# Performance work log

Measured on AMD Instinct MI355X. Metric: run time of the kernel, lower is better.

Reference implementation:

```python
import jax, jax.numpy as jnp
import numpy as np

N, E, F_IN, H, NSE, L, C, G = 50000, 800000, 128, 128, 16, 3, 10, 256


def setup_inputs() -> dict:
    key = jax.random.key(0)
    ks = jax.random.split(key, 32)
    sc = 0.05
    inp = {
        "x": jax.random.normal(ks[0], (N, F_IN), jnp.float32),
        "s": jax.random.normal(ks[1], (N, NSE), jnp.float32),
        "edge_index": jax.random.randint(ks[2], (2, E), 0, N, jnp.int64),
        "batch": jnp.sort(jax.random.randint(ks[3], (N,), 0, G, jnp.int64)),
        # pre: Linear(F_IN, H); embedding_s: Linear(NSE, H)
        "pre_w": jax.random.normal(ks[4], (F_IN, H), jnp.float32) * sc,
        "pre_b": jnp.zeros((H,), jnp.float32),
        "emb_w": jax.random.normal(ks[5], (NSE, H), jnp.float32) * sc,
        "emb_b": jnp.zeros((H,), jnp.float32),
        # per-layer GIN MLP: Linear(2H,H) -> ReLU -> Linear(H,H)
        "gin_w1": jax.random.normal(ks[6], (L, 2 * H, H), jnp.float32) * sc,
        "gin_b1": jnp.zeros((L, H), jnp.float32),
        "gin_w2": jax.random.normal(ks[7], (L, H, H), jnp.float32) * sc,
        "gin_b2": jnp.zeros((L, H), jnp.float32),
        # per-layer GCNConv(H, H)
        "gcn_w": jax.random.normal(ks[8], (L, H, H), jnp.float32) * sc,
        "gcn_b": jnp.zeros((L, H), jnp.float32),
        "whp_w": jax.random.normal(ks[9], (2 * H, H), jnp.float32) * sc,
        "whp_b": jnp.zeros((H,), jnp.float32),
        "post_w": jax.random.normal(ks[10], (H, H), jnp.float32) * sc,
        "post_b": jnp.zeros((H,), jnp.float32),
        "ro_w": jax.random.normal(ks[11], (H, C), jnp.float32) * sc,
        "ro_b": jnp.zeros((C,), jnp.float32),
    }
    return inp


def reference(x, s, edge_index, batch, pre_w, pre_b, emb_w, emb_b,
              gin_w1, gin_b1, gin_w2, gin_b2, gcn_w, gcn_b,
              whp_w, whp_b, post_w, post_b, ro_w, ro_b):
    src, dst = edge_index[0], edge_index[1]
    x = x @ pre_w + pre_b                      # [N, H]
    s = s @ emb_w + emb_b                      # [N, H]
    # GCN symmetric norm with self-loops (deg includes the +1 self loop)
    deg = jax.ops.segment_sum(jnp.ones((E,), x.dtype), dst, num_segments=N) + 1.0
    dinv = jax.lax.rsqrt(deg)                  # [N]
    enorm = (dinv[src] * dinv[dst])[:, None]   # [E, 1]
    self_norm = (dinv * dinv)[:, None]         # [N, 1]
    for i in range(L):
        xc = jnp.concatenate([x, s], axis=-1)  # [N, 2H]
        # GINConv (eps=0): nn(x_i + sum_j x_j)
        agg = jax.ops.segment_sum(xc[src], dst, num_segments=N)
        h = xc + agg
        h = jax.nn.relu(h @ gin_w1[i] + gin_b1[i]) @ gin_w2[i] + gin_b2[i]
        x = jax.nn.relu(h)                     # dropout is identity in eval mode
        # GCNConv on s stream
        hs = s @ gcn_w[i]
        sagg = jax.ops.segment_sum(hs[src] * enorm, dst, num_segments=N)
        s = jnp.tanh(sagg + hs * self_norm + gcn_b[i])
    x = jnp.concatenate([x, s], axis=-1) @ whp_w + whp_b
    g = jax.ops.segment_sum(x, batch, num_segments=G)   # global_add_pool [G, H]
    g = jax.nn.relu(g @ post_w + post_b)
    return jax.nn.log_softmax(g @ ro_w + ro_b, axis=1)
```

## Files before the change

### kernel.cpp

```cpp
#include <hip/hip_runtime.h>
#include <math.h>

typedef __attribute__((ext_vector_type(8))) short short8;
typedef __attribute__((ext_vector_type(4))) float f32x4;
typedef unsigned int uint;
typedef unsigned short ushort;

#define HGRID(n, b) (((n) + (b) - 1) / (b))

__device__ __forceinline__ ushort f2bu(float f) {
    uint x = __builtin_bit_cast(uint, f);
    x = (x + 0x7fffu + ((x >> 16) & 1u)) >> 16;
    return (ushort)x;
}
__device__ __forceinline__ float blo(uint u) {
    return __builtin_bit_cast(float, u << 16);
}
__device__ __forceinline__ float bhi(uint u) {
    return __builtin_bit_cast(float, u & 0xffff0000u);
}
__device__ __forceinline__ uint packbf(float a, float b) {
    return (uint)f2bu(a) | ((uint)f2bu(b) << 16);
}

__device__ __forceinline__ void gload16(const void* g, void* l) {
    __builtin_amdgcn_global_load_lds(
        (const __attribute__((address_space(1))) void*)g,
        (__attribute__((address_space(3))) void*)l, 16, 0, 0);
}


__global__ void count_kernel(const int* __restrict__ dst, int* __restrict__ cnt,
                             int* __restrict__ rank, int E) {
    int e = blockIdx.x * 256 + threadIdx.x;
    if (e < E) rank[e] = atomicAdd(&cnt[dst[e]], 1);
}

__global__ void scan_part(const int* __restrict__ cnt, int* __restrict__ bsum, int N) {
    __shared__ int sh[256];
    int b = blockIdx.x, t = threadIdx.x;
    int base = b * 1024 + t * 4;
    int tsum = 0;
    if (base + 3 < N) {
        int4 v = *(const int4*)(cnt + base);
        tsum = v.x + v.y + v.z + v.w;
    } else {
        #pragma unroll
        for (int k = 0; k < 4; ++k) if (base + k < N) tsum += cnt[base + k];
    }
    sh[t] = tsum;
    __syncthreads();
    for (int d = 128; d > 0; d >>= 1) {
        if (t < d) sh[t] += sh[t + d];
        __syncthreads();
    }
    if (t == 0) bsum[b] = sh[0];
}

__global__ void scan_fill(const int* __restrict__ cnt, const int* __restrict__ bsum,
                          int* __restrict__ offs, float* __restrict__ dinv,
                          int N, int E) {
    __shared__ int sh[256];
    __shared__ int sbase;
    int b = blockIdx.x, t = threadIdx.x;

    if (t < 64) {
        int s = 0;
        for (int i = t; i < b; i += 64) s += bsum[i];
        #pragma unroll
        for (int d = 32; d > 0; d >>= 1) s += __shfl_down(s, d, 64);
        if (t == 0) sbase = s;
    }

    int base = b * 1024 + t * 4;
    int c[4] = {0, 0, 0, 0};
    if (base + 3 < N) {
        int4 v = *(const int4*)(cnt + base);
        c[0] = v.x; c[1] = v.y; c[2] = v.z; c[3] = v.w;
    } else {
        #pragma unroll
        for (int k = 0; k < 4; ++k) if (base + k < N) c[k] = cnt[base + k];
    }
    int tsum = c[0] + c[1] + c[2] + c[3];
    sh[t] = tsum;
    __syncthreads();
    for (int d = 1; d < 256; d <<= 1) {
        int o = (t >= d) ? sh[t - d] : 0;
        __syncthreads();
        sh[t] += o;
        __syncthreads();
    }
    int run = sbase + sh[t] - tsum;
    #pragma unroll
    for (int k = 0; k < 4; ++k) {
        if (base + k < N) {
            offs[base + k] = run;
            dinv[base + k] = rsqrtf((float)c[k] + 1.0f);
            run += c[k];
        }
    }
    if (b == 0 && t == 0) offs[N] = E;
}

__global__ void fill_kernel(const int* __restrict__ src, const int* __restrict__ dst,
                            const int* __restrict__ offs, const int* __restrict__ rank,
                            const float* __restrict__ dinv, int2* __restrict__ epack, int E) {
    int e = blockIdx.x * 256 + threadIdx.x;
    if (e < E) {
        int d = dst[e];
        int sv = src[e];
        epack[offs[d] + rank[e]] = make_int2(sv * 64, __float_as_int(dinv[sv]));
    }
}


struct SetupArgs {
    const float *x, *s;
    const float *pre_w, *pre_b, *emb_w, *emb_b, *gin_w1, *gcn_w, *gin_w2;
    ushort *xs, *Wt_preemb, *Wt_dual, *Wt_gin2;
    float *bias_comb;
    int *cnt; float *gsum; int *cntg;
    int L, N, G;
};

__global__ void setup_kernel(SetupArgs a) {
    long idx = (long)blockIdx.x * 256 + threadIdx.x;
    long nconv = (long)a.N * 24;
    if (idx < nconv) {
        int n = (int)(idx / 24), ch = (int)(idx % 24);
        uint4 o = {0u, 0u, 0u, 0u};
        if (ch < 16) {
            const float4* px = (const float4*)(a.x + (long)n * 128 + ch * 8);
            float4 u = px[0], v = px[1];
            o.x = packbf(u.x, u.y); o.y = packbf(u.z, u.w);
            o.z = packbf(v.x, v.y); o.w = packbf(v.z, v.w);
        } else if (ch < 18) {
            const float4* ps = (const float4*)(a.s + (long)n * 16 + (ch - 16) * 8);
            float4 u = ps[0], v = ps[1];
            o.x = packbf(u.x, u.y); o.y = packbf(u.z, u.w);
            o.z = packbf(v.x, v.y); o.w = packbf(v.z, v.w);
        }
        *(uint4*)(a.xs + idx * 8) = o;
        return;
    }
    idx -= nconv;
    if (idx < 49152) {
        int c = (int)(idx / 192), k = (int)(idx % 192);
        float v = 0.f;
        if (c < 128) { if (k < 128) v = a.pre_w[(long)k * 128 + c]; }
        else if (k >= 128 && k < 144) v = a.emb_w[(long)(k - 128) * 128 + (c - 128)];
        a.Wt_preemb[idx] = f2bu(v);
        return;
    }
    idx -= 49152;
    if (idx < (long)a.L * 65536) {
        int i = (int)(idx / 65536);
        int r = (int)(idx % 65536);
        int c = r / 256, k = r % 256;
        float v = 0.f;
        if (c < 128) v = a.gin_w1[(long)i * 32768 + (long)k * 128 + c];
        else if (k >= 128) v = a.gcn_w[(long)i * 16384 + (long)(k - 128) * 128 + (c - 128)];
        a.Wt_dual[idx] = f2bu(v);
        return;
    }
    idx -= (long)a.L * 65536;
    if (idx < (long)a.L * 16384) {
        int i = (int)(idx / 16384);
        int r = (int)(idx % 16384);
        int c = r / 128, k = r % 128;
        a.Wt_gin2[idx] = f2bu(a.gin_w2[(long)i * 16384 + (long)k * 128 + c]);
        return;
    }
    idx -= (long)a.L * 16384;
    if (idx < 256) { a.bias_comb[idx] = (idx < 128) ? a.pre_b[idx] : a.emb_b[idx - 128]; return; }
    idx -= 256;
    if (idx < a.N) { a.cnt[idx] = 0; return; }
    idx -= a.N;
    if (idx < (long)a.G * 256) { a.gsum[idx] = 0.f; return; }
    idx -= (long)a.G * 256;
    if (idx < a.G) a.cntg[idx] = 0;
}


template<int KPAD, int BN>
__global__ __launch_bounds__(512) void lin_mfma(
    const ushort* __restrict__ A, int a_stride,
    const ushort* __restrict__ Wt, const float* __restrict__ bias,
    ushort* __restrict__ out, int o_stride, int N, int act, int interleaved)
{
    constexpr int BK = 64;
    constexpr int NF = BN / 64;
    __shared__ __align__(16) ushort LA[128][BK];
    __shared__ __align__(16) ushort LB[BN][BK];

    const int tid  = threadIdx.x;
    const int l    = tid & 63;
    const int w    = tid >> 6;
    const int wr   = w >> 2;
    const int wc   = w & 3;
    const int row0 = blockIdx.x * 128;
    const int l15  = l & 15;
    const int lhi  = l >> 4;
    const int lrow = l >> 3;
    const int lslot = l & 7;

    f32x4 acc[4][NF];
    #pragma unroll
    for (int m = 0; m < 4; ++m)
        #pragma unroll
        for (int n = 0; n < NF; ++n) acc[m][n] = (f32x4){0.f, 0.f, 0.f, 0.f};

    for (int k0 = 0; k0 < KPAD; k0 += BK) {
        __syncthreads();
        #pragma unroll
        for (int i = 0; i < 2; ++i) {
            int ci = w * 2 + i;
            int r  = ci * 8 + lrow;
            int gr = row0 + r; if (gr > N - 1) gr = N - 1;
            gload16(A + (long)gr * a_stride + k0 + ((lslot ^ (r & 7)) * 8), &LA[ci * 8][0]);
        }
        #pragma unroll
        for (int i = 0; i < NF; ++i) {
            int ci = w * NF + i;
            int c  = ci * 8 + lrow;
            gload16(Wt + (long)c * KPAD + k0 + ((lslot ^ (c & 7)) * 8), &LB[ci * 8][0]);
        }
        __syncthreads();
        #pragma unroll
        for (int kk = 0; kk < BK; kk += 32) {
            int chb = (kk >> 3) + lhi;
            short8 a[4];
            #pragma unroll
            for (int m = 0; m < 4; ++m) {
                int r = wr * 64 + m * 16 + l15;
                a[m] = *(const short8*)&LA[r][(chb ^ (r & 7)) * 8];
            }
            #pragma unroll
            for (int n = 0; n < NF; ++n) {
                int c = wc * (BN / 4) + n * 16 + l15;
                short8 b = *(const short8*)&LB[c][(chb ^ (c & 7)) * 8];
                #pragma unroll
                for (int m = 0; m < 4; ++m)
                    acc[m][n] = __builtin_amdgcn_mfma_f32_16x16x32_bf16(a[m], b, acc[m][n], 0, 0, 0);
            }
        }
    }

    #pragma unroll
    for (int n = 0; n < NF; ++n) {
        int col = wc * (BN / 4) + n * 16 + l15;
        float bv = bias ? bias[col] : 0.f;
        #pragma unroll
        for (int m = 0; m < 4; ++m) {
            #pragma unroll
            for (int j = 0; j < 4; ++j) {
                int gr = row0 + wr * 64 + m * 16 + (lhi << 2) + j;
                if (gr < N) {
                    float v = acc[m][n][j] + bv;
                    if (act) v = fmaxf(v, 0.f);
                    long off;
                    if (interleaved) {
                        int cc = col & 127;
                        off = (long)gr * 256 + 4 * (cc >> 1) + ((col >> 7) << 1) + (cc & 1);
                    } else {
                        off = (long)gr * o_stride + col;
                    }
                    out[off] = f2bu(v);
                }
            }
        }
    }
}


__global__ __launch_bounds__(256) void fused_gather(
    const uint2* __restrict__ yh, const int* __restrict__ offs,
    const int2* __restrict__ epack,
    const float* __restrict__ dinv,
    const float* __restrict__ b1, const float* __restrict__ gb,
    uint* __restrict__ h1p, uint* __restrict__ xcp, int N)
{
    int node = blockIdx.x * 4 + (threadIdx.x >> 6);
    if (node >= N) return;
    node = __builtin_amdgcn_readfirstlane(node);
    int l = threadIdx.x & 63;

    uint2 self = yh[(long)node * 64 + l];
    float di = dinv[node];
    float g0 = blo(self.x), g1 = bhi(self.x);
    float s0 = 0.f, s1 = 0.f;

    int j0 = __builtin_amdgcn_readfirstlane(offs[node]);
    int j1 = __builtin_amdgcn_readfirstlane(offs[node + 1]);
    int jmid = j0 + ((j1 - j0) & ~15);

    for (int j = j0; j < jmid; j += 16) {
        int2 e[16]; uint2 v[16];
        #pragma unroll
        for (int k = 0; k < 16; ++k) e[k] = epack[j + k];
        #pragma unroll
        for (int k = 0; k < 16; ++k) v[k] = yh[e[k].x + l];
        #pragma unroll
        for (int k = 0; k < 16; ++k) {
            float ds = __int_as_float(e[k].y);
            g0 += blo(v[k].x);
            g1 += bhi(v[k].x);
            s0 += blo(v[k].y) * ds;
            s1 += bhi(v[k].y) * ds;
        }
    }
    for (int j = jmid; j < j1; j += 4) {
        int2 e[4]; uint2 v[4];
        #pragma unroll
        for (int k = 0; k < 4; ++k) {
            int jj = j + k;
            e[k] = epack[(jj < j1) ? jj : (j1 - 1)];
            if (jj >= j1) e[k].y = 0;
        }
        #pragma unroll
        for (int k = 0; k < 4; ++k) v[k] = yh[e[k].x + l];
        #pragma unroll
        for (int k = 0; k < 4; ++k) {
            float ds = __int_as_float(e[k].y);
            float m = (j + k < j1) ? 1.f : 0.f;
            g0 += blo(v[k].x) * m;
            g1 += bhi(v[k].x) * m;
            s0 += blo(v[k].y) * ds;
            s1 += bhi(v[k].y) * ds;
        }
    }

    float2 bb = ((const float2*)b1)[l];
    g0 = fmaxf(g0 + bb.x, 0.f);
    g1 = fmaxf(g1 + bb.y, 0.f);
    h1p[(long)node * 64 + l] = packbf(g0, g1);

    float dii = di * di;
    float2 gg = ((const float2*)gb)[l];
    float t0 = tanhf(s0 * di + blo(self.y) * dii + gg.x);
    float t1 = tanhf(s1 * di + bhi(self.y) * dii + gg.y);
    xcp[(long)node * 128 + 64 + l] = packbf(t0, t1);
}


__global__ void pool_kernel(const ushort* __restrict__ xc, const int* __restrict__ batch,
                            float* __restrict__ gsum, int* __restrict__ cntg, int N) {
    int c  = threadIdx.x;
    int n0 = blockIdx.x * 128;
    if (n0 >= N) return;
    int n1 = min(n0 + 128, N);
    int curg = batch[n0];
    float acc = 0.f;
    int cnt = 0;
    for (int n = n0; n < n1; ++n) {
        int b = batch[n];
        if (b != curg) {
            atomicAdd(&gsum[(long)curg * 256 + c], acc);
            if (c == 0) atomicAdd(&cntg[curg], cnt);
            acc = 0.f; cnt = 0;
            curg = b;
        }
        acc += blo((uint)xc[(long)n * 256 + c]);
        cnt++;
    }
    atomicAdd(&gsum[(long)curg * 256 + c], acc);
    if (c == 0) atomicAdd(&cntg[curg], cnt);
}


__global__ void head_kernel(const float* __restrict__ gsum, const int* __restrict__ cntg,
                            const float* __restrict__ whp_w, const float* __restrict__ whp_b,
                            const float* __restrict__ post_w, const float* __restrict__ post_b,
                            const float* __restrict__ ro_w, const float* __restrict__ ro_b,
                            float* __restrict__ out, int C) {
    __shared__ float row[256];
    __shared__ float xr[128];
    __shared__ float g2[128];
    __shared__ float lg[16];
    __shared__ float s_lse;
    int gi = blockIdx.x;
    int c  = threadIdx.x;
    row[c]       = gsum[(long)gi * 256 + c];
    row[c + 128] = gsum[(long)gi * 256 + 128 + c];
    __syncthreads();
    float cntf = (float)cntg[gi];
    float acc = cntf * whp_b[c];
    for (int k = 0; k < 256; ++k) acc += row[k] * whp_w[(long)k * 128 + c];
    xr[c] = acc;
    __syncthreads();
    float a2 = post_b[c];
    for (int k = 0; k < 128; ++k) a2 += xr[k] * post_w[k * 128 + c];
    g2[c] = fmaxf(a2, 0.f);
    __syncthreads();
    if (c < C) {
        float a = ro_b[c];
        for (int k = 0; k < 128; ++k) a += g2[k] * ro_w[k * C + c];
        lg[c] = a;
    }
    __syncthreads();
    if (c == 0) {
        float m = lg[0];
        for (int i = 1; i < C; ++i) m = fmaxf(m, lg[i]);
        float sum = 0.f;
        for (int i = 0; i < C; ++i) sum += expf(lg[i] - m);
        s_lse = m + logf(sum);
    }
    __syncthreads();
    if (c < C) out[(long)gi * C + c] = lg[c] - s_lse;
}


extern "C" void kernel_launch(void* const* d_in, const int* in_sizes, int n_in,
                              void* d_out, int out_size, void* d_ws, size_t ws_size,
                              hipStream_t stream) {
    const float* x      = (const float*)d_in[0];
    const float* s_in   = (const float*)d_in[1];
    const int*   ei     = (const int*)d_in[2];
    const int*   batch  = (const int*)d_in[3];
    const float* pre_w  = (const float*)d_in[4];
    const float* pre_b  = (const float*)d_in[5];
    const float* emb_w  = (const float*)d_in[6];
    const float* emb_b  = (const float*)d_in[7];
    const float* gin_w1 = (const float*)d_in[8];
    const float* gin_b1 = (const float*)d_in[9];
    const float* gin_w2 = (const float*)d_in[10];
    const float* gin_b2 = (const float*)d_in[11];
    const float* gcn_w  = (const float*)d_in[12];
    const float* gcn_b  = (const float*)d_in[13];
    const float* whp_w  = (const float*)d_in[14];
    const float* whp_b  = (const float*)d_in[15];
    const float* post_w = (const float*)d_in[16];
    const float* post_b = (const float*)d_in[17];
    const float* ro_w   = (const float*)d_in[18];
    const float* ro_b   = (const float*)d_in[19];

    const int H = 128;
    const int N = in_sizes[0] / 128;
    const int E = in_sizes[2] / 2;
    const int C = in_sizes[19];
    const int G = out_size / C;
    const int L = in_sizes[9] / H;

    const int* srcv = ei;
    const int* dstv = ei + E;

    char* p = (char*)d_ws;
    auto alloc = [&](size_t bytes) -> void* {
        void* r = (void*)p;
        p += (bytes + 255) & ~(size_t)255;
        return r;
    };
    ushort* xc   = (ushort*)alloc((size_t)N * 256 * 2);
    ushort* yh   = (ushort*)alloc((size_t)N * 256 * 2);
    ushort* h1   = (ushort*)alloc((size_t)N * 128 * 2);
    ushort* xs   = (ushort*)alloc((size_t)N * 192 * 2);
    ushort* Wt_preemb = (ushort*)alloc(256 * 192 * 2);
    ushort* Wt_dual   = (ushort*)alloc((size_t)L * 256 * 256 * 2);
    ushort* Wt_gin2   = (ushort*)alloc((size_t)L * 128 * 128 * 2);
    float*  bias_comb = (float*)alloc(256 * 4);
    float*  dinv = (float*)alloc((size_t)N * 4);
    float*  gsum = (float*)alloc((size_t)G * 256 * 4);
    int*    cntg = (int*)alloc((size_t)G * 4);
    int* cnt   = (int*)alloc((size_t)N * 4);
    int* offs  = (int*)alloc((size_t)(N + 1) * 4);
    int* rank  = (int*)alloc((size_t)E * 4);
    int* bsum  = (int*)alloc((size_t)HGRID(N, 1024) * 4);
    int2* epack = (int2*)alloc((size_t)E * 8);

    const int nb = HGRID(N, 1024);

    SetupArgs sa;
    sa.x = x; sa.s = s_in;
    sa.pre_w = pre_w; sa.pre_b = pre_b; sa.emb_w = emb_w; sa.emb_b = emb_b;
    sa.gin_w1 = gin_w1; sa.gcn_w = gcn_w; sa.gin_w2 = gin_w2;
    sa.xs = xs; sa.Wt_preemb = Wt_preemb; sa.Wt_dual = Wt_dual; sa.Wt_gin2 = Wt_gin2;
    sa.bias_comb = bias_comb; sa.cnt = cnt; sa.gsum = gsum; sa.cntg = cntg;
    sa.L = L; sa.N = N; sa.G = G;
    long setup_tot = (long)N * 24 + 49152 + (long)L * 65536 + (long)L * 16384 + 256
                   + N + (long)G * 256 + G;
    setup_kernel<<<HGRID(setup_tot, 256), 256, 0, stream>>>(sa);

    count_kernel<<<HGRID(E, 256), 256, 0, stream>>>(dstv, cnt, rank, E);
    scan_part<<<nb, 256, 0, stream>>>(cnt, bsum, N);
    scan_fill<<<nb, 256, 0, stream>>>(cnt, bsum, offs, dinv, N, E);
    fill_kernel<<<HGRID(E, 256), 256, 0, stream>>>(srcv, dstv, offs, rank, dinv, epack, E);

    const int lb = HGRID(N, 128);
    lin_mfma<192, 256><<<lb, 512, 0, stream>>>(xs, 192, Wt_preemb, bias_comb,
                                               xc, 256, N, 0, 0);

    for (int i = 0; i < L; ++i) {
        lin_mfma<256, 256><<<lb, 512, 0, stream>>>(xc, 256, Wt_dual + (size_t)i * 65536,
                                                   nullptr, yh, 256, N, 0, 1);
        fused_gather<<<HGRID(N, 4), 256, 0, stream>>>(
            (const uint2*)yh, offs, epack, dinv,
            gin_b1 + (size_t)i * H, gcn_b + (size_t)i * H,
            (uint*)h1, (uint*)xc, N);
        lin_mfma<128, 128><<<lb, 512, 0, stream>>>(h1, 128, Wt_gin2 + (size_t)i * 16384,
                                                   gin_b2 + (size_t)i * H, xc, 256, N, 1, 0);
    }

    pool_kernel<<<HGRID(N, 128), 256, 0, stream>>>(xc, batch, gsum, cntg, N);
    head_kernel<<<G, 128, 0, stream>>>(gsum, cntg, whp_w, whp_b,
                                       post_w, post_b, ro_w, ro_b, (float*)d_out, C);
}
```

Measured before the change: 394.7 us.

## Fuse GIN second linear with next layer's dual projection in one kernel

Adds a kernel that computes the GIN second linear layer (bias + ReLU) into shared memory and immediately uses it, together with the s half of xc, as input to the next layer's dual projection. The x half of xc is no longer written to global memory and read back between layers, and one launch per layer is removed. The first dual projection is hoisted before the loop and the last layer keeps the original path. The cost is higher shared memory use (about 96 KB per block), which may reduce occupancy, and the x half of xc is left stale for intermediate layers.

```diff
diff --git a/kernel.cpp b/kernel.cpp
--- a/kernel.cpp
+++ b/kernel.cpp
@@ -266,6 +266,161 @@
                         off = (long)gr * o_stride + col;
                     }
                     out[off] = f2bu(v);
+                }
+            }
+        }
+    }
+}
+
+
+__global__ __launch_bounds__(512) void fused_g2d(
+    const ushort* __restrict__ h1,
+    const ushort* __restrict__ xcs,
+    const ushort* __restrict__ Wg2,
+    const float*  __restrict__ b2,
+    const ushort* __restrict__ Wd,
+    ushort* __restrict__ yh, int N)
+{
+    __shared__ __align__(16) ushort XT[128][128];
+    __shared__ __align__(16) ushort SB[256][64];
+    __shared__ __align__(16) ushort SA[128][64];
+
+    const int tid  = threadIdx.x;
+    const int l    = tid & 63;
+    const int w    = tid >> 6;
+    const int wr   = w >> 2;
+    const int wc   = w & 3;
+    const int row0 = blockIdx.x * 128;
+    const int l15  = l & 15;
+    const int lhi  = l >> 4;
+    const int lrow = l >> 3;
+    const int lslot = l & 7;
+
+    f32x4 ax[4][2];
+    #pragma unroll
+    for (int m = 0; m < 4; ++m)
+        #pragma unroll
+        for (int n = 0; n < 2; ++n) ax[m][n] = (f32x4){0.f, 0.f, 0.f, 0.f};
+
+    #pragma unroll
+    for (int k0 = 0; k0 < 128; k0 += 64) {
+        __syncthreads();
+        #pragma unroll
+        for (int i = 0; i < 2; ++i) {
+            int ci = w * 2 + i;
+            int r  = ci * 8 + lrow;
+            int gr = row0 + r; if (gr > N - 1) gr = N - 1;
+            gload16(h1 + (long)gr * 128 + k0 + ((lslot ^ (r & 7)) * 8), &SA[ci * 8][0]);
+        }
+        #pragma unroll
+        for (int i = 0; i < 2; ++i) {
+            int ci = w * 2 + i;
+            int c  = ci * 8 + lrow;
+            gload16(Wg2 + (long)c * 128 + k0 + ((lslot ^ (c & 7)) * 8), &SB[ci * 8][0]);
+        }
+        __syncthreads();
+        #pragma unroll
+        for (int kk = 0; kk < 64; kk += 32) {
+            int chb = (kk >> 3) + lhi;
+            short8 a[4];
+            #pragma unroll
+            for (int m = 0; m < 4; ++m) {
+                int r = wr * 64 + m * 16 + l15;
+                a[m] = *(const short8*)&SA[r][(chb ^ (r & 7)) * 8];
+            }
+            #pragma unroll
+            for (int n = 0; n < 2; ++n) {
+                int c = wc * 32 + n * 16 + l15;
+                short8 b = *(const short8*)&SB[c][(chb ^ (c & 7)) * 8];
+                #pragma unroll
+                for (int m = 0; m < 4; ++m)
+                    ax[m][n] = __builtin_amdgcn_mfma_f32_16x16x32_bf16(a[m], b, ax[m][n], 0, 0, 0);
+            }
+        }
+    }
+    #pragma unroll
+    for (int n = 0; n < 2; ++n) {
+        int col = wc * 32 + n * 16 + l15;
+        float bv = b2[col];
+        #pragma unroll
+        for (int m = 0; m < 4; ++m) {
+            #pragma unroll
+            for (int j = 0; j < 4; ++j) {
+                int row = wr * 64 + m * 16 + (lhi << 2) + j;
+                float v = fmaxf(ax[m][n][j] + bv, 0.f);
+                XT[row][(((col >> 3) ^ (row & 7)) << 3) + (col & 7)] = f2bu(v);
+            }
+        }
+    }
+
+    f32x4 ay[4][4];
+    #pragma unroll
+    for (int m = 0; m < 4; ++m)
+        #pragma unroll
+        for (int n = 0; n < 4; ++n) ay[m][n] = (f32x4){0.f, 0.f, 0.f, 0.f};
+
+    #pragma unroll
+    for (int k0 = 0; k0 < 256; k0 += 64) {
+        __syncthreads();
+        if (k0 >= 128) {
+            #pragma unroll
+            for (int i = 0; i < 2; ++i) {
+                int ci = w * 2 + i;
+                int r  = ci * 8 + lrow;
+                int gr = row0 + r; if (gr > N - 1) gr = N - 1;
+                gload16(xcs + (long)gr * 256 + 128 + (k0 - 128) + ((lslot ^ (r & 7)) * 8),
+                        &SA[ci * 8][0]);
+            }
+        }
+        #pragma unroll
+        for (int i = 0; i < 4; ++i) {
+            int ci = w * 4 + i;
+            int c  = ci * 8 + lrow;
+            gload16(Wd + (long)c * 256 + k0 + ((lslot ^ (c & 7)) * 8), &SB[ci * 8][0]);
+        }
+        __syncthreads();
+        #pragma unroll
+        for (int kk = 0; kk < 64; kk += 32) {
+            short8 a[4];
+            if (k0 < 128) {
+                int chb = ((k0 + kk) >> 3) + lhi;
+                #pragma unroll
+                for (int m = 0; m < 4; ++m) {
+                    int r = wr * 64 + m * 16 + l15;
+                    a[m] = *(const short8*)&XT[r][(chb ^ (r & 7)) * 8];
+                }
+            } else {
+                int chb = (kk >> 3) + lhi;
+                #pragma unroll
+                for (int m = 0; m < 4; ++m) {
+                    int r = wr * 64 + m * 16 + l15;
+                    a[m] = *(const short8*)&SA[r][(chb ^ (r & 7)) * 8];
+                }
+            }
+            int chbb = (kk >> 3) + lhi;
+            #pragma unroll
+            for (int n = 0; n < 4; ++n) {
+                int c = wc * 64 + n * 16 + l15;
+                short8 b = *(const short8*)&SB[c][(chbb ^ (c & 7)) * 8];
+                #pragma unroll
+                for (int m = 0; m < 4; ++m)
+                    ay[m][n] = __builtin_amdgcn_mfma_f32_16x16x32_bf16(a[m], b, ay[m][n], 0, 0, 0);
+            }
+        }
+    }
+
+    #pragma unroll
+    for (int n = 0; n < 4; ++n) {
+        int col = wc * 64 + n * 16 + l15;
+        int cc = col & 127;
+        #pragma unroll
+        for (int m = 0; m < 4; ++m) {
+            #pragma unroll
+            for (int j = 0; j < 4; ++j) {
+                int gr = row0 + wr * 64 + m * 16 + (lhi << 2) + j;
+                if (gr < N) {
+                    long off = (long)gr * 256 + 4 * (cc >> 1) + ((col >> 7) << 1) + (cc & 1);
+                    yh[off] = f2bu(ay[m][n][j]);
                 }
             }
         }
@@ -488,16 +643,21 @@
     const int lb = HGRID(N, 128);
     lin_mfma<192, 256><<<lb, 512, 0, stream>>>(xs, 192, Wt_preemb, bias_comb,
                                                xc, 256, N, 0, 0);
+    lin_mfma<256, 256><<<lb, 512, 0, stream>>>(xc, 256, Wt_dual, nullptr, yh, 256, N, 0, 1);
 
     for (int i = 0; i < L; ++i) {
-        lin_mfma<256, 256><<<lb, 512, 0, stream>>>(xc, 256, Wt_dual + (size_t)i * 65536,
-                                                   nullptr, yh, 256, N, 0, 1);
         fused_gather<<<HGRID(N, 4), 256, 0, stream>>>(
             (const uint2*)yh, offs, epack, dinv,
             gin_b1 + (size_t)i * H, gcn_b + (size_t)i * H,
             (uint*)h1, (uint*)xc, N);
-        lin_mfma<128, 128><<<lb, 512, 0, stream>>>(h1, 128, Wt_gin2 + (size_t)i * 16384,
-                                                   gin_b2 + (size_t)i * H, xc, 256, N, 1, 0);
+        if (i < L - 1) {
+            fused_g2d<<<lb, 512, 0, stream>>>(
+                h1, xc, Wt_gin2 + (size_t)i * 16384, gin_b2 + (size_t)i * H,
+                Wt_dual + (size_t)(i + 1) * 65536, yh, N);
+        } else {
+            lin_mfma<128, 128><<<lb, 512, 0, stream>>>(h1, 128, Wt_gin2 + (size_t)i * 16384,
+                                                       gin_b2 + (size_t)i * H, xc, 256, N, 1, 0);
+        }
     }
 
     pool_kernel<<<HGRID(N, 128), 256, 0, stream>>>(xc, batch, gsum, cntg, N);
```

Measured after the change: 377.8 us. 4.3% less time.
